# Performance work log

Measured on AMD Instinct MI355X. Metric: run time of the kernel, lower is better.

The kernel has to match this reference:

```python
import jax, jax.numpy as jnp
import numpy as np

B, H, S, D = 2, 12, 2048, 64


def setup_inputs() -> dict:
    key = jax.random.key(0)
    kq, kk, kv = jax.random.split(key, 3)
    q = jax.random.normal(kq, (B, H, S, D), dtype=jnp.float32)
    k = jax.random.normal(kk, (B, H, S, D), dtype=jnp.float32)
    v = jax.random.normal(kv, (B, H, S, D), dtype=jnp.float32)
    # causal mask: True = attend (keep), lower triangle
    mask = jnp.tril(jnp.ones((S, S), dtype=bool))
    return {"q": q, "k": k, "v": v, "mask": mask}


def reference(q, k, v, mask):
    dim = q.shape[-1]
    # [B,H,S,S] scores
    scores = jnp.einsum("bhqd,bhkd->bhqk", q, k) / jnp.sqrt(jnp.asarray(dim, q.dtype))
    # dynamic mask-direction logic from the original module:
    # if the mask is denser in the strict upper triangle, True means "mask out";
    # otherwise True means "keep".
    sq = mask.shape[-1]
    sample = mask.reshape(-1, sq, sq)[0]
    upper = jnp.triu(jnp.ones_like(sample, dtype=bool), k=1)
    flip = jnp.sum(sample & upper) > jnp.sum(sample & ~upper)
    keep = jnp.where(flip, ~mask, mask)  # True = keep
    neg_inf = jnp.asarray(-jnp.inf, scores.dtype)
    scores = jnp.where(keep, scores, neg_inf)
    weights = jax.nn.softmax(scores, axis=-1)
    # dropout with p_drop=0.0 is the identity
    return jnp.einsum("bhqk,bhkd->bhqd", weights, v)
```

## Files before the change

kernel.cpp:

```cpp
#include <hip/hip_runtime.h>
#include <hip/hip_bf16.h>


#define SEQ 2048
#define DH 64
#define NHEADS 24
#define BN 64
#define LDK 72
#define ELEMS_PER_TENSOR (NHEADS * SEQ * DH)
#define NSLOT (NHEADS * 16 * 4)
#define WS_KV    ((size_t)2 * ELEMS_PER_TENSOR * 2)
#define WS_FA11  (WS_KV + (size_t)NSLOT * 8192 * 2 + (size_t)NSLOT * 128 * 4)

typedef float f32x4 __attribute__((ext_vector_type(4)));
typedef __bf16 bf16x8 __attribute__((ext_vector_type(8)));
typedef __bf16 bf16x4 __attribute__((ext_vector_type(4)));

#if __has_builtin(__builtin_amdgcn_exp2f)
#define EXP2F(x) __builtin_amdgcn_exp2f(x)
#else
#define EXP2F(x) exp2f(x)
#endif

#define QSCALE 0.1803368801111204f

__global__ __launch_bounds__(256)
void prep_kernel(const float* __restrict__ k, const float* __restrict__ v,
                 __bf16* __restrict__ ks, __bf16* __restrict__ vt)
{
    __shared__ __bf16 T[64][LDK];
    const int bx = blockIdx.x;
    const int tid = threadIdx.x;
    if (bx < 1536) {
        const int idx = (bx * 256 + tid) * 8;
        f32x4 a = *(const f32x4*)(k + idx);
        f32x4 b = *(const f32x4*)(k + idx + 4);
        bf16x8 o;
        #pragma unroll
        for (int j = 0; j < 4; ++j) { o[j] = (__bf16)a[j]; o[4 + j] = (__bf16)b[j]; }
        *(bf16x8*)(ks + idx) = o;
    } else {
        const int b2 = bx - 1536;
        const int bh = b2 >> 5;
        const int s0 = (b2 & 31) * 64;
        const int r = tid >> 2, c0 = (tid & 3) * 16;
        const float* vp = v + (size_t)bh * SEQ * DH + (size_t)(s0 + r) * DH + c0;
        __bf16 tmp[16];
        #pragma unroll
        for (int jj = 0; jj < 16; ++jj) tmp[jj] = (__bf16)vp[jj];
        *(bf16x8*)&T[r][c0]     = *(bf16x8*)&tmp[0];
        *(bf16x8*)&T[r][c0 + 8] = *(bf16x8*)&tmp[8];
        __syncthreads();
        const int d = tid >> 2, j0 = (tid & 3) * 16;
        __bf16 o[16];
        #pragma unroll
        for (int jj = 0; jj < 16; ++jj) o[jj] = T[j0 + jj][d];
        __bf16* op = vt + (size_t)bh * DH * SEQ + (size_t)d * SEQ + s0 + j0;
        *(bf16x8*)op       = *(bf16x8*)&o[0];
        *(bf16x8*)(op + 8) = *(bf16x8*)&o[8];
    }
}

__global__ __launch_bounds__(256, 3)
void fa11_kernel(const float* __restrict__ q, const __bf16* __restrict__ ks,
                 const __bf16* __restrict__ vt,
                 __bf16* __restrict__ opart, float* __restrict__ lpart,
                 float* __restrict__ out)
{
    const int bx = blockIdx.x;
    const int xcd = bx & 7;
    const int sub = bx >> 3;
    const int bh = (sub / 40) * 8 + xcd;
    const int rem = 39 - (sub % 40);
    int mt2, st;
    if      (rem >= 36) { mt2 = 15; st = 36; }
    else if (rem >= 32) { mt2 = 14; st = 32; }
    else if (rem >= 28) { mt2 = 13; st = 28; }
    else if (rem >= 24) { mt2 = 12; st = 24; }
    else if (rem >= 21) { mt2 = 11; st = 21; }
    else if (rem >= 18) { mt2 = 10; st = 18; }
    else if (rem >= 15) { mt2 = 9;  st = 15; }
    else if (rem >= 12) { mt2 = 8;  st = 12; }
    else if (rem >= 10) { mt2 = 7;  st = 10; }
    else if (rem >= 8)  { mt2 = 6;  st = 8; }
    else if (rem >= 6)  { mt2 = 5;  st = 6; }
    else if (rem >= 4)  { mt2 = 4;  st = 4; }
    else                { mt2 = rem; st = rem; }
    const int chunk = rem - st;
    const int jt0 = chunk * 8;
    const int jt_end = min(jt0 + 8, 2 * mt2 + 2);
    const int q0 = mt2 * 128;

    const int tid = threadIdx.x;
    const int w = tid >> 6, lane = tid & 63;
    const int g = lane >> 4, li = lane & 15;

    __shared__ __bf16 Ks[2][64 * 64];
    __shared__ __bf16 Vs[2][64 * 64];
    __shared__ __bf16 Ps[4 * 32 * 64];

    const __bf16* kh = ks + (size_t)bh * SEQ * DH;
    const __bf16* vh = vt + (size_t)bh * DH * SEQ;

    bf16x8 qf[2][2];
    #pragma unroll
    for (int a = 0; a < 2; ++a) {
        const float* qp = q + (size_t)bh * SEQ * DH +
                          (size_t)(q0 + w * 32 + a * 16 + li) * DH + g * 8;
        #pragma unroll
        for (int c = 0; c < 2; ++c) {
            f32x4 x0 = *(const f32x4*)(qp + c * 32);
            f32x4 x1 = *(const f32x4*)(qp + c * 32 + 4);
            #pragma unroll
            for (int j = 0; j < 4; ++j) {
                qf[a][c][j]     = (__bf16)(x0[j] * QSCALE);
                qf[a][c][4 + j] = (__bf16)(x1[j] * QSCALE);
            }
        }
    }

    bf16x8 ones;
    #pragma unroll
    for (int j = 0; j < 8; ++j) ones[j] = (__bf16)1.0f;

    f32x4 acc[2][4] = {};
    f32x4 accl[2] = {};

    const int srow0 = tid >> 3;
    const int sg    = tid & 7;

    bf16x8 kr[2], vr[2];
    #pragma unroll
    for (int s = 0; s < 2; ++s) {
        const int row = s * 32 + srow0;
        const int lg = sg ^ (row & 7);
        kr[s] = *(const bf16x8*)(kh + (size_t)(jt0 * BN + row) * DH + lg * 8);
        vr[s] = *(const bf16x8*)(vh + (size_t)row * SEQ + jt0 * BN + lg * 8);
    }
    #pragma unroll
    for (int s = 0; s < 2; ++s) {
        *(bf16x8*)((char*)Ks[0] + s * 4096 + tid * 16) = kr[s];
        *(bf16x8*)((char*)Vs[0] + s * 4096 + tid * 16) = vr[s];
    }
    if (jt0 + 1 < jt_end) {
        const int kv1 = (jt0 + 1) * BN;
        #pragma unroll
        for (int s = 0; s < 2; ++s) {
            const int row = s * 32 + srow0;
            const int lg = sg ^ (row & 7);
            kr[s] = *(const bf16x8*)(kh + (size_t)(kv1 + row) * DH + lg * 8);
            vr[s] = *(const bf16x8*)(vh + (size_t)row * SEQ + kv1 + lg * 8);
        }
    }
    __syncthreads();

    int buf = 0;
    for (int jt = jt0; jt < jt_end; ++jt) {
        if (jt + 1 < jt_end) {
            #pragma unroll
            for (int s = 0; s < 2; ++s) {
                *(bf16x8*)((char*)Ks[buf ^ 1] + s * 4096 + tid * 16) = kr[s];
                *(bf16x8*)((char*)Vs[buf ^ 1] + s * 4096 + tid * 16) = vr[s];
            }
        }
        if (jt + 2 < jt_end) {
            const int kv2 = (jt + 2) * BN;
            #pragma unroll
            for (int s = 0; s < 2; ++s) {
                const int row = s * 32 + srow0;
                const int lg = sg ^ (row & 7);
                kr[s] = *(const bf16x8*)(kh + (size_t)(kv2 + row) * DH + lg * 8);
                vr[s] = *(const bf16x8*)(vh + (size_t)row * SEQ + kv2 + lg * 8);
            }
        }

        const char* Kb = (const char*)Ks[buf];
        const char* Vb = (const char*)Vs[buf];
        float s4[2][4][4];
        #pragma unroll
        for (int t = 0; t < 4; ++t) {
            f32x4 sa0 = {}, sa1 = {};
            #pragma unroll
            for (int c = 0; c < 2; ++c) {
                bf16x8 kf = *(const bf16x8*)(Kb +
                    (t * 16 + li) * 128 + (((c * 4 + g) ^ (li & 7)) << 4));
                sa0 = __builtin_amdgcn_mfma_f32_16x16x32_bf16(kf, qf[0][c], sa0, 0, 0, 0);
                sa1 = __builtin_amdgcn_mfma_f32_16x16x32_bf16(kf, qf[1][c], sa1, 0, 0, 0);
            }
            #pragma unroll
            for (int r = 0; r < 4; ++r) { s4[0][t][r] = sa0[r]; s4[1][t][r] = sa1[r]; }
        }

        if (jt >= 2 * mt2) {
            #pragma unroll
            for (int a = 0; a < 2; ++a) {
                const int qr = q0 + w * 32 + a * 16 + li;
                #pragma unroll
                for (int t = 0; t < 4; ++t) {
                    #pragma unroll
                    for (int r = 0; r < 4; ++r)
                        if (jt * 64 + t * 16 + g * 4 + r > qr) s4[a][t][r] = -1e30f;
                }
            }
        }

        #pragma unroll
        for (int a = 0; a < 2; ++a) {
            const int row = a * 16 + li;
            #pragma unroll
            for (int t = 0; t < 4; ++t) {
                bf16x4 p4;
                #pragma unroll
                for (int r = 0; r < 4; ++r) p4[r] = (__bf16)EXP2F(s4[a][t][r]);
                const int pg = (t * 2 + (g >> 1)) ^ (li & 7);
                *(bf16x4*)((char*)Ps + w * 4096 + row * 128 + (pg << 4) + ((g & 1) << 3)) = p4;
            }
        }

        #pragma unroll
        for (int c = 0; c < 2; ++c) {
            const int pgp = ((c * 4 + g) ^ (li & 7)) << 4;
            bf16x8 pf0 = *(const bf16x8*)((const char*)Ps + w * 4096 + li * 128 + pgp);
            bf16x8 pf1 = *(const bf16x8*)((const char*)Ps + w * 4096 + (16 + li) * 128 + pgp);
            accl[0] = __builtin_amdgcn_mfma_f32_16x16x32_bf16(pf0, ones, accl[0], 0, 0, 0);
            accl[1] = __builtin_amdgcn_mfma_f32_16x16x32_bf16(pf1, ones, accl[1], 0, 0, 0);
            #pragma unroll
            for (int t = 0; t < 4; ++t) {
                bf16x8 vf = *(const bf16x8*)(Vb + (t * 16 + li) * 128 + pgp);
                acc[0][t] = __builtin_amdgcn_mfma_f32_16x16x32_bf16(pf0, vf, acc[0][t], 0, 0, 0);
                acc[1][t] = __builtin_amdgcn_mfma_f32_16x16x32_bf16(pf1, vf, acc[1][t], 0, 0, 0);
            }
        }

        if (jt + 1 < jt_end) __syncthreads();
        buf ^= 1;
    }

    if (2 * mt2 + 2 <= 8) {
        float* oh = out + (size_t)bh * SEQ * DH;
        #pragma unroll
        for (int a = 0; a < 2; ++a) {
            #pragma unroll
            for (int r = 0; r < 4; ++r) {
                const int row = q0 + w * 32 + a * 16 + g * 4 + r;
                const float inv = 1.0f / accl[a][r];
                float* op = oh + (size_t)row * DH + li;
                #pragma unroll
                for (int t = 0; t < 4; ++t) op[t * 16] = acc[a][t][r] * inv;
            }
        }
    } else {
        const int slot = (bh * 16 + mt2) * 4 + chunk;
        __bf16* po = opart + (size_t)slot * 8192;
        #pragma unroll
        for (int a = 0; a < 2; ++a) {
            #pragma unroll
            for (int r = 0; r < 4; ++r) {
                const int row = w * 32 + a * 16 + g * 4 + r;
                __bf16* op = po + row * 64 + li;
                #pragma unroll
                for (int t = 0; t < 4; ++t) op[t * 16] = (__bf16)acc[a][t][r];
                if (li == 0) lpart[(size_t)slot * 128 + row] = accl[a][r];
            }
        }
    }
}

__global__ __launch_bounds__(256)
void fa_reduce(const __bf16* __restrict__ opart, const float* __restrict__ lpart,
               float* __restrict__ out)
{
    const int bx = blockIdx.x;
    const int xcd = bx & 7;
    const int r2 = bx >> 3;
    const int bh = (r2 / 12) * 8 + xcd;
    const int mt2 = 4 + (r2 % 12);
    const int nc = (mt2 >> 2) + 1;
    const int base = (bh * 16 + mt2) * 4;
    const int tid = threadIdx.x;
    #pragma unroll
    for (int rnd = 0; rnd < 8; ++rnd) {
        const int flat = rnd * 1024 + tid * 4;
        const int row = flat >> 6;
        float o0 = 0, o1 = 0, o2 = 0, o3 = 0, l = 0;
        for (int c = 0; c < nc; ++c) {
            bf16x4 ov = *(const bf16x4*)(opart + (size_t)(base + c) * 8192 + flat);
            o0 += (float)ov[0]; o1 += (float)ov[1]; o2 += (float)ov[2]; o3 += (float)ov[3];
            l += lpart[(size_t)(base + c) * 128 + row];
        }
        const float inv = 1.0f / l;
        f32x4 res = { o0 * inv, o1 * inv, o2 * inv, o3 * inv };
        *(f32x4*)(out + (size_t)bh * SEQ * DH + (size_t)mt2 * 8192 + flat) = res;
    }
}

__global__ __launch_bounds__(256, 2)
void fa_causal_kernel(const float* __restrict__ q, const float* __restrict__ k,
                      const float* __restrict__ v, float* __restrict__ out)
{
    const int mt = 31 - (blockIdx.x & 31);
    const int bh = blockIdx.x >> 5;
    const int tid = threadIdx.x;
    const int w = tid >> 6, lane = tid & 63;
    const int g = lane >> 4, li = lane & 15;
    const int m0 = mt * 64;
    __shared__ __bf16 KsF[BN][LDK];
    __shared__ __bf16 VsF[DH][LDK];
    __shared__ __bf16 PsF[4][16][LDK];
    const size_t head_off = (size_t)bh * SEQ * DH;
    const float* qh = q + head_off;
    const float* kh = k + head_off;
    const float* vh = v + head_off;
    float* oh = out + head_off;
    const int qrow = m0 + w * 16 + li;
    bf16x8 qf[2];
    {
        const float* qp = qh + (size_t)qrow * DH + g * 8;
        #pragma unroll
        for (int c = 0; c < 2; ++c) {
            const float* p = qp + c * 32;
            #pragma unroll
            for (int jj = 0; jj < 8; ++jj) qf[c][jj] = (__bf16)p[jj];
        }
    }
    f32x4 acc[4] = {};
    float mrow[4], lrow[4];
    #pragma unroll
    for (int r = 0; r < 4; ++r) { mrow[r] = -1e30f; lrow[r] = 0.0f; }
    const float scale = 0.125f;
    const int srow = tid >> 2, scol = (tid & 3) * 16;
    for (int jt = 0; jt <= mt; ++jt) {
        const int kv0 = jt * BN;
        __syncthreads();
        {
            const float* kp = kh + (size_t)(kv0 + srow) * DH + scol;
            __bf16 tmp[16];
            #pragma unroll
            for (int jj = 0; jj < 16; ++jj) tmp[jj] = (__bf16)kp[jj];
            *(bf16x8*)&KsF[srow][scol]     = *(bf16x8*)&tmp[0];
            *(bf16x8*)&KsF[srow][scol + 8] = *(bf16x8*)&tmp[8];
            const float* vp = vh + (size_t)(kv0 + srow) * DH + scol;
            #pragma unroll
            for (int jj = 0; jj < 16; ++jj) VsF[scol + jj][srow] = (__bf16)vp[jj];
        }
        __syncthreads();
        float s4[4][4];
        #pragma unroll
        for (int t = 0; t < 4; ++t) {
            f32x4 sa = {};
            #pragma unroll
            for (int c = 0; c < 2; ++c) {
                bf16x8 kfr = *(const bf16x8*)&KsF[t * 16 + li][c * 32 + g * 8];
                sa = __builtin_amdgcn_mfma_f32_16x16x32_bf16(qf[c], kfr, sa, 0, 0, 0);
            }
            #pragma unroll
            for (int r = 0; r < 4; ++r) s4[t][r] = sa[r] * scale;
        }
        if (jt == mt) {
            #pragma unroll
            for (int t = 0; t < 4; ++t) {
                const int col = kv0 + t * 16 + li;
                #pragma unroll
                for (int r = 0; r < 4; ++r)
                    if (col > m0 + w * 16 + g * 4 + r) s4[t][r] = -1e30f;
            }
        }
        #pragma unroll
        for (int r = 0; r < 4; ++r) {
            float mx = fmaxf(fmaxf(s4[0][r], s4[1][r]), fmaxf(s4[2][r], s4[3][r]));
            #pragma unroll
            for (int off = 1; off < 16; off <<= 1)
                mx = fmaxf(mx, __shfl_xor(mx, off, 64));
            const float mnew = fmaxf(mrow[r], mx);
            const float alpha = __expf(mrow[r] - mnew);
            mrow[r] = mnew;
            float ps = 0.0f;
            #pragma unroll
            for (int t = 0; t < 4; ++t) {
                const float p = __expf(s4[t][r] - mnew);
                s4[t][r] = p;
                ps += p;
            }
            #pragma unroll
            for (int off = 1; off < 16; off <<= 1)
                ps += __shfl_xor(ps, off, 64);
            lrow[r] = lrow[r] * alpha + ps;
            #pragma unroll
            for (int t = 0; t < 4; ++t) acc[t][r] *= alpha;
        }
        #pragma unroll
        for (int t = 0; t < 4; ++t)
            #pragma unroll
            for (int r = 0; r < 4; ++r)
                PsF[w][g * 4 + r][t * 16 + li] = (__bf16)s4[t][r];
        __syncthreads();
        #pragma unroll
        for (int c = 0; c < 2; ++c) {
            bf16x8 pf = *(const bf16x8*)&PsF[w][li][c * 32 + g * 8];
            #pragma unroll
            for (int t = 0; t < 4; ++t) {
                bf16x8 vfr = *(const bf16x8*)&VsF[t * 16 + li][c * 32 + g * 8];
                acc[t] = __builtin_amdgcn_mfma_f32_16x16x32_bf16(pf, vfr, acc[t], 0, 0, 0);
            }
        }
    }
    #pragma unroll
    for (int r = 0; r < 4; ++r) {
        const int row = m0 + w * 16 + g * 4 + r;
        const float inv = 1.0f / lrow[r];
        float* op = oh + (size_t)row * DH + li;
        #pragma unroll
        for (int t = 0; t < 4; ++t) op[t * 16] = acc[t][r] * inv;
    }
}

extern "C" void kernel_launch(void* const* d_in, const int* in_sizes, int n_in,
                              void* d_out, int out_size, void* d_ws, size_t ws_size,
                              hipStream_t stream) {
    (void)in_sizes; (void)n_in; (void)out_size;
    const float* q = (const float*)d_in[0];
    const float* k = (const float*)d_in[1];
    const float* v = (const float*)d_in[2];
    float* out = (float*)d_out;

    if (ws_size >= WS_FA11) {
        __bf16* ks = (__bf16*)d_ws;
        __bf16* vt = ks + ELEMS_PER_TENSOR;
        __bf16* opart = (__bf16*)((char*)d_ws + WS_KV);
        float* lpart = (float*)((char*)d_ws + WS_KV + (size_t)NSLOT * 8192 * 2);
        prep_kernel<<<dim3(1536 + 768), dim3(256), 0, stream>>>(k, v, ks, vt);
        fa11_kernel<<<dim3(960), dim3(256), 0, stream>>>(q, ks, vt, opart, lpart, out);
        fa_reduce<<<dim3(288), dim3(256), 0, stream>>>(opart, lpart, out);
    } else {
        fa_causal_kernel<<<dim3(NHEADS * 32), dim3(256), 0, stream>>>(q, k, v, out);
    }
}
```

Baseline: 131.8 us.

## Fuse split-KV reduction into attention kernel via last-block atomic counter

Removes the separate fa_reduce launch. Each split chunk writes its partial output, then bumps a per-group atomic counter, and the last block to finish does the combine and final normalization. The counters are zeroed in the prep kernel. This saves one kernel launch and its tail, at the cost of extra fences, an atomic per block, and uneven work for the last block of each group.

```diff
diff --git a/kernel.cpp b/kernel.cpp
--- a/kernel.cpp
+++ b/kernel.cpp
@@ -9,8 +9,10 @@
 #define LDK 72
 #define ELEMS_PER_TENSOR (NHEADS * SEQ * DH)
 #define NSLOT (NHEADS * 16 * 4)
+#define NGROUP (NHEADS * 16)
 #define WS_KV    ((size_t)2 * ELEMS_PER_TENSOR * 2)
 #define WS_FA11  (WS_KV + (size_t)NSLOT * 8192 * 2 + (size_t)NSLOT * 128 * 4)
+#define WS_FA12  (WS_FA11 + (size_t)NGROUP * 4)
 
 typedef float f32x4 __attribute__((ext_vector_type(4)));
 typedef __bf16 bf16x8 __attribute__((ext_vector_type(8)));
@@ -26,11 +28,15 @@
 
 __global__ __launch_bounds__(256)
 void prep_kernel(const float* __restrict__ k, const float* __restrict__ v,
-                 __bf16* __restrict__ ks, __bf16* __restrict__ vt)
+                 __bf16* __restrict__ ks, __bf16* __restrict__ vt,
+                 int* __restrict__ cnt)
 {
     __shared__ __bf16 T[64][LDK];
     const int bx = blockIdx.x;
     const int tid = threadIdx.x;
+    if (bx == 0) {
+        for (int i = tid; i < NGROUP; i += 256) cnt[i] = 0;
+    }
     if (bx < 1536) {
         const int idx = (bx * 256 + tid) * 8;
         f32x4 a = *(const f32x4*)(k + idx);
@@ -65,7 +71,7 @@
 void fa11_kernel(const float* __restrict__ q, const __bf16* __restrict__ ks,
                  const __bf16* __restrict__ vt,
                  __bf16* __restrict__ opart, float* __restrict__ lpart,
-                 float* __restrict__ out)
+                 float* __restrict__ out, int* __restrict__ cnt)
 {
     const int bx = blockIdx.x;
     const int xcd = bx & 7;
@@ -98,6 +104,7 @@
     __shared__ __bf16 Ks[2][64 * 64];
     __shared__ __bf16 Vs[2][64 * 64];
     __shared__ __bf16 Ps[4 * 32 * 64];
+    __shared__ int is_last;
 
     const __bf16* kh = ks + (size_t)bh * SEQ * DH;
     const __bf16* vh = vt + (size_t)bh * DH * SEQ;
@@ -250,7 +257,8 @@
             }
         }
     } else {
-        const int slot = (bh * 16 + mt2) * 4 + chunk;
+        const int group = bh * 16 + mt2;
+        const int slot = group * 4 + chunk;
         __bf16* po = opart + (size_t)slot * 8192;
         #pragma unroll
         for (int a = 0; a < 2; ++a) {
@@ -263,34 +271,31 @@
                 if (li == 0) lpart[(size_t)slot * 128 + row] = accl[a][r];
             }
         }
-    }
-}
-
-__global__ __launch_bounds__(256)
-void fa_reduce(const __bf16* __restrict__ opart, const float* __restrict__ lpart,
-               float* __restrict__ out)
-{
-    const int bx = blockIdx.x;
-    const int xcd = bx & 7;
-    const int r2 = bx >> 3;
-    const int bh = (r2 / 12) * 8 + xcd;
-    const int mt2 = 4 + (r2 % 12);
-    const int nc = (mt2 >> 2) + 1;
-    const int base = (bh * 16 + mt2) * 4;
-    const int tid = threadIdx.x;
-    #pragma unroll
-    for (int rnd = 0; rnd < 8; ++rnd) {
-        const int flat = rnd * 1024 + tid * 4;
-        const int row = flat >> 6;
-        float o0 = 0, o1 = 0, o2 = 0, o3 = 0, l = 0;
-        for (int c = 0; c < nc; ++c) {
-            bf16x4 ov = *(const bf16x4*)(opart + (size_t)(base + c) * 8192 + flat);
-            o0 += (float)ov[0]; o1 += (float)ov[1]; o2 += (float)ov[2]; o3 += (float)ov[3];
-            l += lpart[(size_t)(base + c) * 128 + row];
-        }
-        const float inv = 1.0f / l;
-        f32x4 res = { o0 * inv, o1 * inv, o2 * inv, o3 * inv };
-        *(f32x4*)(out + (size_t)bh * SEQ * DH + (size_t)mt2 * 8192 + flat) = res;
+
+        const int nc = (mt2 >> 2) + 1;
+        __threadfence();
+        __syncthreads();
+        if (tid == 0)
+            is_last = (atomicAdd(&cnt[group], 1) == nc - 1);
+        __syncthreads();
+        if (is_last) {
+            __threadfence();
+            const int base = group * 4;
+            #pragma unroll
+            for (int rnd = 0; rnd < 8; ++rnd) {
+                const int flat = rnd * 1024 + tid * 4;
+                const int row = flat >> 6;
+                float o0 = 0, o1 = 0, o2 = 0, o3 = 0, l = 0;
+                for (int c = 0; c < nc; ++c) {
+                    bf16x4 ov = *(const bf16x4*)(opart + (size_t)(base + c) * 8192 + flat);
+                    o0 += (float)ov[0]; o1 += (float)ov[1]; o2 += (float)ov[2]; o3 += (float)ov[3];
+                    l += lpart[(size_t)(base + c) * 128 + row];
+                }
+                const float inv = 1.0f / l;
+                f32x4 res = { o0 * inv, o1 * inv, o2 * inv, o3 * inv };
+                *(f32x4*)(out + (size_t)bh * SEQ * DH + (size_t)mt2 * 8192 + flat) = res;
+            }
+        }
     }
 }
 
@@ -423,14 +428,14 @@
     const float* v = (const float*)d_in[2];
     float* out = (float*)d_out;
 
-    if (ws_size >= WS_FA11) {
+    if (ws_size >= WS_FA12) {
         __bf16* ks = (__bf16*)d_ws;
         __bf16* vt = ks + ELEMS_PER_TENSOR;
         __bf16* opart = (__bf16*)((char*)d_ws + WS_KV);
         float* lpart = (float*)((char*)d_ws + WS_KV + (size_t)NSLOT * 8192 * 2);
-        prep_kernel<<<dim3(1536 + 768), dim3(256), 0, stream>>>(k, v, ks, vt);
-        fa11_kernel<<<dim3(960), dim3(256), 0, stream>>>(q, ks, vt, opart, lpart, out);
-        fa_reduce<<<dim3(288), dim3(256), 0, stream>>>(opart, lpart, out);
+        int* cnt = (int*)((char*)d_ws + WS_FA11);
+        prep_kernel<<<dim3(1536 + 768), dim3(256), 0, stream>>>(k, v, ks, vt, cnt);
+        fa11_kernel<<<dim3(960), dim3(256), 0, stream>>>(q, ks, vt, opart, lpart, out, cnt);
     } else {
         fa_causal_kernel<<<dim3(NHEADS * 32), dim3(256), 0, stream>>>(q, k, v, out);
     }
```

Result: slower. 276.0 us (+109.4%).

## Drop LDS staging of K/V tiles; load MFMA operands directly from global

Applied to the files above, without the earlier changes.

Removes the double-buffered shared-memory staging of K and V tiles and the per-iteration barrier. Each wave now reads its MFMA K and V fragments straight from global memory, relying on L1/L2 to serve the reuse across the four waves. Freeing the LDS and registers allows raising the occupancy hint to 4 blocks per CU. The trade-off is that each tile is fetched four times from cache instead of once. The loads are also no longer prefetched ahead of the compute, so memory latency may be exposed.

```diff
diff --git a/kernel.cpp b/kernel.cpp
--- a/kernel.cpp
+++ b/kernel.cpp
@@ -61,8 +61,8 @@
     }
 }
 
-__global__ __launch_bounds__(256, 3)
-void fa11_kernel(const float* __restrict__ q, const __bf16* __restrict__ ks,
+__global__ __launch_bounds__(256, 4)
+void fa13_kernel(const float* __restrict__ q, const __bf16* __restrict__ ks,
                  const __bf16* __restrict__ vt,
                  __bf16* __restrict__ opart, float* __restrict__ lpart,
                  float* __restrict__ out)
@@ -95,8 +95,6 @@
     const int w = tid >> 6, lane = tid & 63;
     const int g = lane >> 4, li = lane & 15;
 
-    __shared__ __bf16 Ks[2][64 * 64];
-    __shared__ __bf16 Vs[2][64 * 64];
     __shared__ __bf16 Ps[4 * 32 * 64];
 
     const __bf16* kh = ks + (size_t)bh * SEQ * DH;
@@ -126,64 +124,15 @@
     f32x4 acc[2][4] = {};
     f32x4 accl[2] = {};
 
-    const int srow0 = tid >> 3;
-    const int sg    = tid & 7;
-
-    bf16x8 kr[2], vr[2];
-    #pragma unroll
-    for (int s = 0; s < 2; ++s) {
-        const int row = s * 32 + srow0;
-        const int lg = sg ^ (row & 7);
-        kr[s] = *(const bf16x8*)(kh + (size_t)(jt0 * BN + row) * DH + lg * 8);
-        vr[s] = *(const bf16x8*)(vh + (size_t)row * SEQ + jt0 * BN + lg * 8);
-    }
-    #pragma unroll
-    for (int s = 0; s < 2; ++s) {
-        *(bf16x8*)((char*)Ks[0] + s * 4096 + tid * 16) = kr[s];
-        *(bf16x8*)((char*)Vs[0] + s * 4096 + tid * 16) = vr[s];
-    }
-    if (jt0 + 1 < jt_end) {
-        const int kv1 = (jt0 + 1) * BN;
-        #pragma unroll
-        for (int s = 0; s < 2; ++s) {
-            const int row = s * 32 + srow0;
-            const int lg = sg ^ (row & 7);
-            kr[s] = *(const bf16x8*)(kh + (size_t)(kv1 + row) * DH + lg * 8);
-            vr[s] = *(const bf16x8*)(vh + (size_t)row * SEQ + kv1 + lg * 8);
-        }
-    }
-    __syncthreads();
-
-    int buf = 0;
     for (int jt = jt0; jt < jt_end; ++jt) {
-        if (jt + 1 < jt_end) {
-            #pragma unroll
-            for (int s = 0; s < 2; ++s) {
-                *(bf16x8*)((char*)Ks[buf ^ 1] + s * 4096 + tid * 16) = kr[s];
-                *(bf16x8*)((char*)Vs[buf ^ 1] + s * 4096 + tid * 16) = vr[s];
-            }
-        }
-        if (jt + 2 < jt_end) {
-            const int kv2 = (jt + 2) * BN;
-            #pragma unroll
-            for (int s = 0; s < 2; ++s) {
-                const int row = s * 32 + srow0;
-                const int lg = sg ^ (row & 7);
-                kr[s] = *(const bf16x8*)(kh + (size_t)(kv2 + row) * DH + lg * 8);
-                vr[s] = *(const bf16x8*)(vh + (size_t)row * SEQ + kv2 + lg * 8);
-            }
-        }
-
-        const char* Kb = (const char*)Ks[buf];
-        const char* Vb = (const char*)Vs[buf];
+        const __bf16* kt = kh + (size_t)jt * (BN * DH);
         float s4[2][4][4];
         #pragma unroll
         for (int t = 0; t < 4; ++t) {
             f32x4 sa0 = {}, sa1 = {};
             #pragma unroll
             for (int c = 0; c < 2; ++c) {
-                bf16x8 kf = *(const bf16x8*)(Kb +
-                    (t * 16 + li) * 128 + (((c * 4 + g) ^ (li & 7)) << 4));
+                bf16x8 kf = *(const bf16x8*)(kt + (t * 16 + li) * DH + (c * 4 + g) * 8);
                 sa0 = __builtin_amdgcn_mfma_f32_16x16x32_bf16(kf, qf[0][c], sa0, 0, 0, 0);
                 sa1 = __builtin_amdgcn_mfma_f32_16x16x32_bf16(kf, qf[1][c], sa1, 0, 0, 0);
             }
@@ -226,14 +175,12 @@
             accl[1] = __builtin_amdgcn_mfma_f32_16x16x32_bf16(pf1, ones, accl[1], 0, 0, 0);
             #pragma unroll
             for (int t = 0; t < 4; ++t) {
-                bf16x8 vf = *(const bf16x8*)(Vb + (t * 16 + li) * 128 + pgp);
+                bf16x8 vf = *(const bf16x8*)(vh + (size_t)(t * 16 + li) * SEQ +
+                                             jt * BN + (c * 4 + g) * 8);
                 acc[0][t] = __builtin_amdgcn_mfma_f32_16x16x32_bf16(pf0, vf, acc[0][t], 0, 0, 0);
                 acc[1][t] = __builtin_amdgcn_mfma_f32_16x16x32_bf16(pf1, vf, acc[1][t], 0, 0, 0);
             }
         }
-
-        if (jt + 1 < jt_end) __syncthreads();
-        buf ^= 1;
     }
 
     if (2 * mt2 + 2 <= 8) {
@@ -429,7 +376,7 @@
         __bf16* opart = (__bf16*)((char*)d_ws + WS_KV);
         float* lpart = (float*)((char*)d_ws + WS_KV + (size_t)NSLOT * 8192 * 2);
         prep_kernel<<<dim3(1536 + 768), dim3(256), 0, stream>>>(k, v, ks, vt);
-        fa11_kernel<<<dim3(960), dim3(256), 0, stream>>>(q, ks, vt, opart, lpart, out);
+        fa13_kernel<<<dim3(960), dim3(256), 0, stream>>>(q, ks, vt, opart, lpart, out);
         fa_reduce<<<dim3(288), dim3(256), 0, stream>>>(opart, lpart, out);
     } else {
         fa_causal_kernel<<<dim3(NHEADS * 32), dim3(256), 0, stream>>>(q, k, v, out);
```

Measured after the change: 167.6 us. 1.27x slower.
